# Kernel tuning notes

Measured on AMD Instinct MI355X. Metric: run time of the kernel, lower is better.

The kernel has to match this reference:

```python
import jax, jax.numpy as jnp
import numpy as np

N = 100000
E = 1600000
IN_C = 512
OUT_C = 128


def setup_inputs() -> dict:
    key = jax.random.key(0)
    k1, k2, k3, k4 = jax.random.split(key, 4)
    x = jax.random.normal(k1, (N, IN_C), dtype=jnp.float32)
    edge_index = jax.random.randint(k2, (2, E), 0, N, dtype=jnp.int64)
    # GCNConv parameters (glorot weight, zero bias as in PyG defaults)
    scale = jnp.sqrt(6.0 / (IN_C + OUT_C)).astype(jnp.float32)
    W = jax.random.uniform(k3, (IN_C, OUT_C), dtype=jnp.float32, minval=-scale, maxval=scale)
    b = jnp.zeros((OUT_C,), dtype=jnp.float32)
    return {"x": x, "edge_index": edge_index, "W": W, "b": b}


def reference(x, edge_index, W, b):
    n = x.shape[0]
    loops = jnp.arange(n, dtype=edge_index.dtype)
    src = jnp.concatenate([edge_index[0], loops])  # [E+N] message sources
    dst = jnp.concatenate([edge_index[1], loops])  # [E+N] message targets
    # symmetric GCN normalization: deg over targets incl. self-loops
    deg = jax.ops.segment_sum(jnp.ones_like(src, dtype=x.dtype), dst, num_segments=n)
    dinv = jnp.where(deg > 0, jax.lax.rsqrt(deg), 0.0)
    norm = dinv[src] * dinv[dst]  # [E+N]
    h = x @ W  # [N, OUT_C] transform first (in > out)
    msg = h[src] * norm[:, None]  # [E+N, OUT_C]
    out = jax.ops.segment_sum(msg, dst, num_segments=n) + b
    return (out, 0)
```

## Files before the change

kernel.cpp:

```cpp
#include <hip/hip_runtime.h>

#define IN_C 512
#define OUT_C 128
#define SCAN_TILE 2048
#define NB 128
#define CHUNK 8192

typedef float f32x4 __attribute__((ext_vector_type(4)));
typedef __bf16 bf16x8 __attribute__((ext_vector_type(8)));

static inline int cdiv(int a, int b) { return (a + b - 1) / b; }

__device__ __forceinline__ unsigned short bfbits(__bf16 h) {
  return __builtin_bit_cast(unsigned short, h);
}


__global__ __launch_bounds__(256) void hist_kernel(const int* __restrict__ dst,
                                                   int* __restrict__ table,
                                                   int nchunks, int E) {
  __shared__ int hcnt[NB];
  int t = threadIdx.x;
  int c = blockIdx.x;
  if (t < NB) hcnt[t] = 0;
  __syncthreads();
  int base = c * CHUNK;
  for (int i = t; i < CHUNK; i += 256) {
    int e = base + i;
    if (e < E) atomicAdd(&hcnt[dst[e] >> 10], 1);
  }
  __syncthreads();
  if (t < NB) table[t * nchunks + c] = hcnt[t];
}

__global__ __launch_bounds__(256) void tscan_kernel(int* __restrict__ table,
                                                    int* __restrict__ bstart,
                                                    int nchunks, int E) {
  __shared__ int sh[256];
  int t = threadIdx.x;
  int total = NB * nchunks;
  int S = (total + 255) / 256;
  int lo = t * S;
  int hi = lo + S; if (hi > total) hi = total;
  int s = 0;
  int i = lo;
  for (; i + 4 <= hi; i += 4)
    s += table[i] + table[i + 1] + table[i + 2] + table[i + 3];
  for (; i < hi; i++) s += table[i];
  sh[t] = s;
  __syncthreads();
  for (int off = 1; off < 256; off <<= 1) {
    int x = sh[t];
    if (t >= off) x += sh[t - off];
    __syncthreads();
    sh[t] = x;
    __syncthreads();
  }
  int run = sh[t] - s;
  for (i = lo; i < hi; i++) {
    int v = table[i];
    table[i] = run;
    run += v;
  }
  __syncthreads();
  for (int b = t; b < NB; b += 256) bstart[b] = table[b * nchunks];
  if (t == 0) bstart[NB] = E;
}

__global__ __launch_bounds__(256) void scat2_kernel(const int* __restrict__ src,
                                                    const int* __restrict__ dst,
                                                    const int* __restrict__ table,
                                                    int2* __restrict__ inter,
                                                    int nchunks, int E) {
  __shared__ int cur[NB];
  int t = threadIdx.x;
  int c = blockIdx.x;
  if (t < NB) cur[t] = table[t * nchunks + c];
  __syncthreads();
  int base = c * CHUNK;
  for (int i = t; i < CHUNK; i += 256) {
    int e = base + i;
    if (e < E) {
      int d = dst[e];
      int pos = atomicAdd(&cur[d >> 10], 1);
      inter[pos] = make_int2(src[e], d);
    }
  }
}

__global__ __launch_bounds__(256) void bdeg_kernel(const int2* __restrict__ inter,
                                                   const int* __restrict__ bstart,
                                                   int* __restrict__ deg, int n) {
  __shared__ int dl[1024];
  int t = threadIdx.x;
  int b = blockIdx.x;
  for (int i = t; i < 1024; i += 256) dl[i] = 0;
  __syncthreads();
  int lo = bstart[b], hi = bstart[b + 1];
  for (int e = lo + t; e < hi; e += 256) atomicAdd(&dl[inter[e].y & 1023], 1);
  __syncthreads();
  int nb0 = b << 10;
  for (int i = t; i < 1024; i += 256) {
    int node = nb0 + i;
    if (node < n) deg[node] = dl[i];
  }
}

__global__ __launch_bounds__(256) void dinv_kernel(const int* __restrict__ deg,
                                                   float* __restrict__ dinv, int n) {
  int i = blockIdx.x * 256 + threadIdx.x;
  if (i < n) dinv[i] = rsqrtf((float)deg[i] + 1.0f);
}

__global__ __launch_bounds__(256) void scan1_kernel(const int* __restrict__ deg,
                                                    int* __restrict__ offs,
                                                    int* __restrict__ bsums, int n) {
  __shared__ int sh[256];
  int t = threadIdx.x;
  int base = blockIdx.x * SCAN_TILE + t * 8;
  int v[8];
  int s = 0;
#pragma unroll
  for (int i = 0; i < 8; i++) {
    int idx = base + i;
    v[i] = (idx < n) ? deg[idx] : 0;
    s += v[i];
  }
  sh[t] = s;
  __syncthreads();
  for (int off = 1; off < 256; off <<= 1) {
    int x = sh[t];
    if (t >= off) x += sh[t - off];
    __syncthreads();
    sh[t] = x;
    __syncthreads();
  }
  int run = sh[t] - s;
#pragma unroll
  for (int i = 0; i < 8; i++) {
    int idx = base + i;
    if (idx < n) offs[idx] = run;
    run += v[i];
  }
  if (t == 255) bsums[blockIdx.x] = sh[255];
}

__global__ __launch_bounds__(256) void scan2_kernel(int* __restrict__ bsums, int nb) {
  __shared__ int sh[256];
  int t = threadIdx.x;
  int v = (t < nb) ? bsums[t] : 0;
  sh[t] = v;
  __syncthreads();
  for (int off = 1; off < 256; off <<= 1) {
    int x = sh[t];
    if (t >= off) x += sh[t - off];
    __syncthreads();
    sh[t] = x;
    __syncthreads();
  }
  if (t < nb) bsums[t] = sh[t] - v;
}

__global__ __launch_bounds__(256) void scan3_kernel(int* __restrict__ offs,
                                                    const int* __restrict__ bsums,
                                                    int n, int E) {
  int i = blockIdx.x * 256 + threadIdx.x;
  if (i < n) offs[i] = offs[i] + bsums[i >> 11];
  if (i == 0) offs[n] = E;
}

__global__ __launch_bounds__(256) void scat3_kernel(const int2* __restrict__ inter,
                                                    const int* __restrict__ bstart,
                                                    const int* __restrict__ offs,
                                                    int* __restrict__ csr_src, int n) {
  __shared__ int cur[1024];
  int t = threadIdx.x;
  int b = blockIdx.x;
  int nb0 = b << 10;
  for (int i = t; i < 1024; i += 256) {
    int node = nb0 + i;
    cur[i] = (node < n) ? offs[node] : 0;
  }
  __syncthreads();
  int lo = bstart[b], hi = bstart[b + 1];
  for (int e = lo + t; e < hi; e += 256) {
    int2 sd = inter[e];
    int pos = atomicAdd(&cur[sd.y & 1023], 1);
    csr_src[pos] = sd.x;
  }
}

__global__ __launch_bounds__(256) void wsplit_kernel(const float* __restrict__ W,
                                                     unsigned short* __restrict__ wfh,
                                                     unsigned short* __restrict__ wfl) {
  int i = blockIdx.x * 256 + threadIdx.x;
  if (i >= IN_C * OUT_C) return;
  int k = i >> 7;
  int col = i & 127;
  float w = W[i];
  __bf16 hb = (__bf16)w;
  __bf16 lb = (__bf16)(w - (float)hb);
  int ks = k >> 5;
  int lg = (k & 31) >> 3;
  int j = k & 7;
  int cb = col >> 4;
  int lane = lg * 16 + (col & 15);
  size_t idx = ((size_t)(ks * 8 + cb) * 64 + lane) * 8 + j;
  wfh[idx] = bfbits(hb);
  wfl[idx] = bfbits(lb);
}

__global__ __launch_bounds__(256) void gemm_mfma_kernel(
    const float* __restrict__ x, const unsigned short* __restrict__ wfh,
    const unsigned short* __restrict__ wfl, unsigned short* __restrict__ h, int n) {
  __shared__ float xs[2][4096];

  const int tid = threadIdx.x;
  const int wv = tid >> 6;
  const int lane = tid & 63;
  const int l15 = lane & 15;
  const int lg = lane >> 4;
  const int wr = wv >> 1;
  const int wc = wv & 1;
  const int row0 = blockIdx.x * 128;

  const float* gsrc[4];
#pragma unroll
  for (int i = 0; i < 4; i++) {
    int pslot = i * 256 + tid;
    int row = pslot >> 3;
    int q = pslot & 7;
    int s = q ^ (row & 7);
    int grow = row0 + row;
    if (grow > n - 1) grow = n - 1;
    gsrc[i] = x + (size_t)grow * IN_C + s * 4;
  }

  const unsigned short* bph = wfh + ((size_t)(wc * 4) * 64 + lane) * 8;
  const unsigned short* bpl = wfl + ((size_t)(wc * 4) * 64 + lane) * 8;

  f32x4 acc[4][4];
#pragma unroll
  for (int i = 0; i < 4; i++)
#pragma unroll
    for (int j = 0; j < 4; j++) acc[i][j] = (f32x4)0.0f;

#pragma unroll
  for (int i = 0; i < 4; i++) {
    char* lp = (char*)&xs[0][0] + i * 4096 + wv * 1024;
    __builtin_amdgcn_global_load_lds(
        (const __attribute__((address_space(1))) void*)gsrc[i],
        (__attribute__((address_space(3))) void*)lp, 16, 0, 0);
    gsrc[i] += 32;
  }
  __syncthreads();

  int cur = 0;
  for (int ks = 0; ks < 16; ks++) {
    if (ks < 15) {
#pragma unroll
      for (int i = 0; i < 4; i++) {
        char* lp = (char*)&xs[cur ^ 1][0] + i * 4096 + wv * 1024;
        __builtin_amdgcn_global_load_lds(
            (const __attribute__((address_space(1))) void*)gsrc[i],
            (__attribute__((address_space(3))) void*)lp, 16, 0, 0);
        gsrc[i] += 32;
      }
    }
    bf16x8 bh[4], bl[4];
#pragma unroll
    for (int nt = 0; nt < 4; nt++) {
      bh[nt] = __builtin_bit_cast(bf16x8, *(const uint4*)(bph + (size_t)ks * 4096 + nt * 512));
      bl[nt] = __builtin_bit_cast(bf16x8, *(const uint4*)(bpl + (size_t)ks * 4096 + nt * 512));
    }
    const float* bp = &xs[cur][0];
    bf16x8 ah[4];
#pragma unroll
    for (int rt = 0; rt < 4; rt++) {
      int row = wr * 64 + rt * 16 + l15;
      int r7 = row & 7;
      int s0 = (lg * 2) ^ r7;
      int s1 = (lg * 2 + 1) ^ r7;
      float4 f0 = *(const float4*)(bp + row * 32 + s0 * 4);
      float4 f1 = *(const float4*)(bp + row * 32 + s1 * 4);
      float f[8] = {f0.x, f0.y, f0.z, f0.w, f1.x, f1.y, f1.z, f1.w};
      bf16x8 hh;
#pragma unroll
      for (int j = 0; j < 8; j++) hh[j] = (__bf16)f[j];
      ah[rt] = hh;
    }
#pragma unroll
    for (int rt = 0; rt < 4; rt++)
#pragma unroll
      for (int nt = 0; nt < 4; nt++) {
        acc[rt][nt] = __builtin_amdgcn_mfma_f32_16x16x32_bf16(ah[rt], bh[nt], acc[rt][nt], 0, 0, 0);
        acc[rt][nt] = __builtin_amdgcn_mfma_f32_16x16x32_bf16(ah[rt], bl[nt], acc[rt][nt], 0, 0, 0);
      }
    __syncthreads();
    cur ^= 1;
  }

#pragma unroll
  for (int rt = 0; rt < 4; rt++) {
    int rowbase = row0 + wr * 64 + rt * 16 + lg * 4;
#pragma unroll
    for (int nt = 0; nt < 4; nt++) {
      int col = wc * 64 + nt * 16 + l15;
#pragma unroll
      for (int r = 0; r < 4; r++) {
        int row = rowbase + r;
        if (row < n) h[(size_t)row * OUT_C + col] = bfbits((__bf16)acc[rt][nt][r]);
      }
    }
  }
}

__device__ __forceinline__ float bflo(unsigned int u) {
  return __builtin_bit_cast(float, u << 16);
}
__device__ __forceinline__ float bfhi(unsigned int u) {
  return __builtin_bit_cast(float, u & 0xffff0000u);
}

__global__ __launch_bounds__(256) void gather_kernel(const int* __restrict__ offs,
                                                     const int* __restrict__ csr_src,
                                                     const unsigned short* __restrict__ h,
                                                     const float* __restrict__ dinv,
                                                     const float* __restrict__ b,
                                                     float* __restrict__ out,
                                                     int n, int tail) {
  int wid = threadIdx.x >> 6;
  int lane = threadIdx.x & 63;
  int l15 = lane & 15;
  int q = lane >> 4;
  int node = blockIdx.x * 4 + wid;
  if (node >= n) return;

  int start = offs[node];
  int end = offs[node + 1];

  float ax0 = 0, ay0 = 0, ax1 = 0, ay1 = 0, ax2 = 0, ay2 = 0, ax3 = 0, ay3 = 0;

  int e = start + q;
  for (; e + 4 < end; e += 8) {
    int s0 = csr_src[e];
    int s1 = csr_src[e + 4];
    float w0 = dinv[s0];
    float w1 = dinv[s1];
    uint4 u0 = *(const uint4*)(h + (size_t)s0 * OUT_C + l15 * 8);
    uint4 u1 = *(const uint4*)(h + (size_t)s1 * OUT_C + l15 * 8);
    ax0 += bflo(u0.x) * w0 + bflo(u1.x) * w1;
    ay0 += bfhi(u0.x) * w0 + bfhi(u1.x) * w1;
    ax1 += bflo(u0.y) * w0 + bflo(u1.y) * w1;
    ay1 += bfhi(u0.y) * w0 + bfhi(u1.y) * w1;
    ax2 += bflo(u0.z) * w0 + bflo(u1.z) * w1;
    ay2 += bfhi(u0.z) * w0 + bfhi(u1.z) * w1;
    ax3 += bflo(u0.w) * w0 + bflo(u1.w) * w1;
    ay3 += bfhi(u0.w) * w0 + bfhi(u1.w) * w1;
  }
  if (e < end) {
    int s0 = csr_src[e];
    float w0 = dinv[s0];
    uint4 u0 = *(const uint4*)(h + (size_t)s0 * OUT_C + l15 * 8);
    ax0 += bflo(u0.x) * w0; ay0 += bfhi(u0.x) * w0;
    ax1 += bflo(u0.y) * w0; ay1 += bfhi(u0.y) * w0;
    ax2 += bflo(u0.z) * w0; ay2 += bfhi(u0.z) * w0;
    ax3 += bflo(u0.w) * w0; ay3 += bfhi(u0.w) * w0;
  }

#pragma unroll
  for (int mask = 16; mask <= 32; mask <<= 1) {
    ax0 += __shfl_xor(ax0, mask); ay0 += __shfl_xor(ay0, mask);
    ax1 += __shfl_xor(ax1, mask); ay1 += __shfl_xor(ay1, mask);
    ax2 += __shfl_xor(ax2, mask); ay2 += __shfl_xor(ay2, mask);
    ax3 += __shfl_xor(ax3, mask); ay3 += __shfl_xor(ay3, mask);
  }

  float dd = dinv[node];
  uint4 us = *(const uint4*)(h + (size_t)node * OUT_C + l15 * 8);
  ax0 = (ax0 + bflo(us.x) * dd) * dd; ay0 = (ay0 + bfhi(us.x) * dd) * dd;
  ax1 = (ax1 + bflo(us.y) * dd) * dd; ay1 = (ay1 + bfhi(us.y) * dd) * dd;
  ax2 = (ax2 + bflo(us.z) * dd) * dd; ay2 = (ay2 + bfhi(us.z) * dd) * dd;
  ax3 = (ax3 + bflo(us.w) * dd) * dd; ay3 = (ay3 + bfhi(us.w) * dd) * dd;

  if (q == 0) {
    float4 b0 = *(const float4*)(b + l15 * 8);
    float4 b1 = *(const float4*)(b + l15 * 8 + 4);
    float4 o0 = make_float4(ax0 + b0.x, ay0 + b0.y, ax1 + b0.z, ay1 + b0.w);
    float4 o1 = make_float4(ax2 + b1.x, ay2 + b1.y, ax3 + b1.z, ay3 + b1.w);
    float* op = out + (size_t)node * OUT_C + l15 * 8;
    *(float4*)op = o0;
    *(float4*)(op + 4) = o1;
  }

  if (node == 0 && lane == 0) {
    for (int t = 0; t < tail; t++) out[(size_t)n * OUT_C + t] = 0.0f;
  }
}

extern "C" void kernel_launch(void* const* d_in, const int* in_sizes, int n_in,
                              void* d_out, int out_size, void* d_ws, size_t ws_size,
                              hipStream_t stream) {
  const float* x = (const float*)d_in[0];
  const int* ei = (const int*)d_in[1];
  const float* W = (const float*)d_in[2];
  const float* b = (const float*)d_in[3];

  const int n = in_sizes[0] / IN_C;
  const int E = in_sizes[1] / 2;
  const int* src = ei;
  const int* dst = ei + E;
  float* out = (float*)d_out;

  const int nchunks = cdiv(E, CHUNK);
  const int nbk = cdiv(n, 1024);

  size_t p = 0;
  auto alloc = [&](size_t bytes) { size_t o = p; p += (bytes + 255) & ~(size_t)255; return o; };
  char* ws = (char*)d_ws;
  float*          dinv   = (float*)(ws + alloc((size_t)n * 4));
  int*            offs   = (int*)(ws + alloc(((size_t)n + 1) * 4));
  int*            csrsrc = (int*)(ws + alloc((size_t)E * 4));
  int*            deg    = (int*)(ws + alloc((size_t)n * 4));
  int*            bsums  = (int*)(ws + alloc(256 * 4));
  int*            bstart = (int*)(ws + alloc((NB + 1) * 4));
  unsigned short* wfh    = (unsigned short*)(ws + alloc((size_t)IN_C * OUT_C * 2));
  unsigned short* wfl    = (unsigned short*)(ws + alloc((size_t)IN_C * OUT_C * 2));
  size_t upos = p;
  int2*           inter  = (int2*)(ws + upos);
  int*            table  = (int*)(ws + upos + (((size_t)E * 8 + 255) & ~(size_t)255));
  unsigned short* h      = (unsigned short*)(ws + upos);

  const int nb = cdiv(n, SCAN_TILE);

  wsplit_kernel<<<cdiv(IN_C * OUT_C, 256), 256, 0, stream>>>(W, wfh, wfl);
  hist_kernel<<<nchunks, 256, 0, stream>>>(dst, table, nchunks, E);
  tscan_kernel<<<1, 256, 0, stream>>>(table, bstart, nchunks, E);
  scat2_kernel<<<nchunks, 256, 0, stream>>>(src, dst, table, inter, nchunks, E);
  bdeg_kernel<<<nbk, 256, 0, stream>>>(inter, bstart, deg, n);
  dinv_kernel<<<cdiv(n, 256), 256, 0, stream>>>(deg, dinv, n);
  scan1_kernel<<<nb, 256, 0, stream>>>(deg, offs, bsums, n);
  scan2_kernel<<<1, 256, 0, stream>>>(bsums, nb);
  scan3_kernel<<<cdiv(n, 256), 256, 0, stream>>>(offs, bsums, n, E);
  scat3_kernel<<<nbk, 256, 0, stream>>>(inter, bstart, offs, csrsrc, n);
  gemm_mfma_kernel<<<cdiv(n, 128), 256, 0, stream>>>(x, wfh, wfl, h, n);
  int tail = out_size - n * OUT_C;
  gather_kernel<<<cdiv(n, 4), 256, 0, stream>>>(offs, csrsrc, h, dinv, b, out, n, tail);
}
```

Baseline: 277.6 us.

## Fuse degree, dinv and offset scan into bucket kernel; prescale h by dinv

Measured after the change: 268.4 us. 1.03x faster.

```diff
diff --git a/kernel.cpp b/kernel.cpp
--- a/kernel.cpp
+++ b/kernel.cpp
@@ -2,7 +2,6 @@
 
 #define IN_C 512
 #define OUT_C 128
-#define SCAN_TILE 2048
 #define NB 128
 #define CHUNK 8192
 
@@ -70,7 +69,7 @@
 __global__ __launch_bounds__(256) void scat2_kernel(const int* __restrict__ src,
                                                     const int* __restrict__ dst,
                                                     const int* __restrict__ table,
-                                                    int2* __restrict__ inter,
+                                                    int* __restrict__ inter,
                                                     int nchunks, int E) {
   __shared__ int cur[NB];
   int t = threadIdx.x;
@@ -83,48 +82,31 @@
     if (e < E) {
       int d = dst[e];
       int pos = atomicAdd(&cur[d >> 10], 1);
-      inter[pos] = make_int2(src[e], d);
-    }
-  }
-}
-
-__global__ __launch_bounds__(256) void bdeg_kernel(const int2* __restrict__ inter,
-                                                   const int* __restrict__ bstart,
-                                                   int* __restrict__ deg, int n) {
+      inter[pos] = (src[e] << 10) | (d & 1023);
+    }
+  }
+}
+
+__global__ __launch_bounds__(256) void bdeg_offs_kernel(const int* __restrict__ inter,
+                                                        const int* __restrict__ bstart,
+                                                        int* __restrict__ offs,
+                                                        float* __restrict__ dinv,
+                                                        int n, int E, int nbk) {
   __shared__ int dl[1024];
+  __shared__ int sh[256];
   int t = threadIdx.x;
   int b = blockIdx.x;
   for (int i = t; i < 1024; i += 256) dl[i] = 0;
   __syncthreads();
   int lo = bstart[b], hi = bstart[b + 1];
-  for (int e = lo + t; e < hi; e += 256) atomicAdd(&dl[inter[e].y & 1023], 1);
-  __syncthreads();
-  int nb0 = b << 10;
-  for (int i = t; i < 1024; i += 256) {
-    int node = nb0 + i;
-    if (node < n) deg[node] = dl[i];
-  }
-}
-
-__global__ __launch_bounds__(256) void dinv_kernel(const int* __restrict__ deg,
-                                                   float* __restrict__ dinv, int n) {
-  int i = blockIdx.x * 256 + threadIdx.x;
-  if (i < n) dinv[i] = rsqrtf((float)deg[i] + 1.0f);
-}
-
-__global__ __launch_bounds__(256) void scan1_kernel(const int* __restrict__ deg,
-                                                    int* __restrict__ offs,
-                                                    int* __restrict__ bsums, int n) {
-  __shared__ int sh[256];
-  int t = threadIdx.x;
-  int base = blockIdx.x * SCAN_TILE + t * 8;
-  int v[8];
+  for (int e = lo + t; e < hi; e += 256) atomicAdd(&dl[inter[e] & 1023], 1);
+  __syncthreads();
+  int c[4];
   int s = 0;
 #pragma unroll
-  for (int i = 0; i < 8; i++) {
-    int idx = base + i;
-    v[i] = (idx < n) ? deg[idx] : 0;
-    s += v[i];
+  for (int j = 0; j < 4; j++) {
+    c[j] = dl[t * 4 + j];
+    s += c[j];
   }
   sh[t] = s;
   __syncthreads();
@@ -135,41 +117,21 @@
     sh[t] = x;
     __syncthreads();
   }
-  int run = sh[t] - s;
-#pragma unroll
-  for (int i = 0; i < 8; i++) {
-    int idx = base + i;
-    if (idx < n) offs[idx] = run;
-    run += v[i];
-  }
-  if (t == 255) bsums[blockIdx.x] = sh[255];
-}
-
-__global__ __launch_bounds__(256) void scan2_kernel(int* __restrict__ bsums, int nb) {
-  __shared__ int sh[256];
-  int t = threadIdx.x;
-  int v = (t < nb) ? bsums[t] : 0;
-  sh[t] = v;
-  __syncthreads();
-  for (int off = 1; off < 256; off <<= 1) {
-    int x = sh[t];
-    if (t >= off) x += sh[t - off];
-    __syncthreads();
-    sh[t] = x;
-    __syncthreads();
-  }
-  if (t < nb) bsums[t] = sh[t] - v;
-}
-
-__global__ __launch_bounds__(256) void scan3_kernel(int* __restrict__ offs,
-                                                    const int* __restrict__ bsums,
-                                                    int n, int E) {
-  int i = blockIdx.x * 256 + threadIdx.x;
-  if (i < n) offs[i] = offs[i] + bsums[i >> 11];
-  if (i == 0) offs[n] = E;
-}
-
-__global__ __launch_bounds__(256) void scat3_kernel(const int2* __restrict__ inter,
+  int run = sh[t] - s + lo;
+  int nb0 = b << 10;
+#pragma unroll
+  for (int j = 0; j < 4; j++) {
+    int node = nb0 + t * 4 + j;
+    if (node < n) {
+      offs[node] = run;
+      dinv[node] = rsqrtf((float)c[j] + 1.0f);
+    }
+    run += c[j];
+  }
+  if (b == nbk - 1 && t == 255) offs[n] = E;
+}
+
+__global__ __launch_bounds__(256) void scat3_kernel(const int* __restrict__ inter,
                                                     const int* __restrict__ bstart,
                                                     const int* __restrict__ offs,
                                                     int* __restrict__ csr_src, int n) {
@@ -184,9 +146,9 @@
   __syncthreads();
   int lo = bstart[b], hi = bstart[b + 1];
   for (int e = lo + t; e < hi; e += 256) {
-    int2 sd = inter[e];
-    int pos = atomicAdd(&cur[sd.y & 1023], 1);
-    csr_src[pos] = sd.x;
+    int u = inter[e];
+    int pos = atomicAdd(&cur[u & 1023], 1);
+    csr_src[pos] = u >> 10;
   }
 }
 
@@ -212,7 +174,8 @@
 
 __global__ __launch_bounds__(256) void gemm_mfma_kernel(
     const float* __restrict__ x, const unsigned short* __restrict__ wfh,
-    const unsigned short* __restrict__ wfl, unsigned short* __restrict__ h, int n) {
+    const unsigned short* __restrict__ wfl, const float* __restrict__ dinv,
+    unsigned short* __restrict__ h, int n) {
   __shared__ float xs[2][4096];
 
   const int tid = threadIdx.x;
@@ -304,12 +267,15 @@
   for (int rt = 0; rt < 4; rt++) {
     int rowbase = row0 + wr * 64 + rt * 16 + lg * 4;
 #pragma unroll
-    for (int nt = 0; nt < 4; nt++) {
-      int col = wc * 64 + nt * 16 + l15;
-#pragma unroll
-      for (int r = 0; r < 4; r++) {
-        int row = rowbase + r;
-        if (row < n) h[(size_t)row * OUT_C + col] = bfbits((__bf16)acc[rt][nt][r]);
+    for (int r = 0; r < 4; r++) {
+      int row = rowbase + r;
+      if (row < n) {
+        float di = dinv[row];
+#pragma unroll
+        for (int nt = 0; nt < 4; nt++) {
+          int col = wc * 64 + nt * 16 + l15;
+          h[(size_t)row * OUT_C + col] = bfbits((__bf16)(acc[rt][nt][r] * di));
+        }
       }
     }
   }
@@ -345,27 +311,20 @@
   for (; e + 4 < end; e += 8) {
     int s0 = csr_src[e];
     int s1 = csr_src[e + 4];
-    float w0 = dinv[s0];
-    float w1 = dinv[s1];
     uint4 u0 = *(const uint4*)(h + (size_t)s0 * OUT_C + l15 * 8);
     uint4 u1 = *(const uint4*)(h + (size_t)s1 * OUT_C + l15 * 8);
-    ax0 += bflo(u0.x) * w0 + bflo(u1.x) * w1;
-    ay0 += bfhi(u0.x) * w0 + bfhi(u1.x) * w1;
-    ax1 += bflo(u0.y) * w0 + bflo(u1.y) * w1;
-    ay1 += bfhi(u0.y) * w0 + bfhi(u1.y) * w1;
-    ax2 += bflo(u0.z) * w0 + bflo(u1.z) * w1;
-    ay2 += bfhi(u0.z) * w0 + bfhi(u1.z) * w1;
-    ax3 += bflo(u0.w) * w0 + bflo(u1.w) * w1;
-    ay3 += bfhi(u0.w) * w0 + bfhi(u1.w) * w1;
+    ax0 += bflo(u0.x) + bflo(u1.x); ay0 += bfhi(u0.x) + bfhi(u1.x);
+    ax1 += bflo(u0.y) + bflo(u1.y); ay1 += bfhi(u0.y) + bfhi(u1.y);
+    ax2 += bflo(u0.z) + bflo(u1.z); ay2 += bfhi(u0.z) + bfhi(u1.z);
+    ax3 += bflo(u0.w) + bflo(u1.w); ay3 += bfhi(u0.w) + bfhi(u1.w);
   }
   if (e < end) {
     int s0 = csr_src[e];
-    float w0 = dinv[s0];
     uint4 u0 = *(const uint4*)(h + (size_t)s0 * OUT_C + l15 * 8);
-    ax0 += bflo(u0.x) * w0; ay0 += bfhi(u0.x) * w0;
-    ax1 += bflo(u0.y) * w0; ay1 += bfhi(u0.y) * w0;
-    ax2 += bflo(u0.z) * w0; ay2 += bfhi(u0.z) * w0;
-    ax3 += bflo(u0.w) * w0; ay3 += bfhi(u0.w) * w0;
+    ax0 += bflo(u0.x); ay0 += bfhi(u0.x);
+    ax1 += bflo(u0.y); ay1 += bfhi(u0.y);
+    ax2 += bflo(u0.z); ay2 += bfhi(u0.z);
+    ax3 += bflo(u0.w); ay3 += bfhi(u0.w);
   }
 
 #pragma unroll
@@ -378,10 +337,10 @@
 
   float dd = dinv[node];
   uint4 us = *(const uint4*)(h + (size_t)node * OUT_C + l15 * 8);
-  ax0 = (ax0 + bflo(us.x) * dd) * dd; ay0 = (ay0 + bfhi(us.x) * dd) * dd;
-  ax1 = (ax1 + bflo(us.y) * dd) * dd; ay1 = (ay1 + bfhi(us.y) * dd) * dd;
-  ax2 = (ax2 + bflo(us.z) * dd) * dd; ay2 = (ay2 + bfhi(us.z) * dd) * dd;
-  ax3 = (ax3 + bflo(us.w) * dd) * dd; ay3 = (ay3 + bfhi(us.w) * dd) * dd;
+  ax0 = (ax0 + bflo(us.x)) * dd; ay0 = (ay0 + bfhi(us.x)) * dd;
+  ax1 = (ax1 + bflo(us.y)) * dd; ay1 = (ay1 + bfhi(us.y)) * dd;
+  ax2 = (ax2 + bflo(us.z)) * dd; ay2 = (ay2 + bfhi(us.z)) * dd;
+  ax3 = (ax3 + bflo(us.w)) * dd; ay3 = (ay3 + bfhi(us.w)) * dd;
 
   if (q == 0) {
     float4 b0 = *(const float4*)(b + l15 * 8);
@@ -421,29 +380,21 @@
   float*          dinv   = (float*)(ws + alloc((size_t)n * 4));
   int*            offs   = (int*)(ws + alloc(((size_t)n + 1) * 4));
   int*            csrsrc = (int*)(ws + alloc((size_t)E * 4));
-  int*            deg    = (int*)(ws + alloc((size_t)n * 4));
-  int*            bsums  = (int*)(ws + alloc(256 * 4));
   int*            bstart = (int*)(ws + alloc((NB + 1) * 4));
   unsigned short* wfh    = (unsigned short*)(ws + alloc((size_t)IN_C * OUT_C * 2));
   unsigned short* wfl    = (unsigned short*)(ws + alloc((size_t)IN_C * OUT_C * 2));
   size_t upos = p;
-  int2*           inter  = (int2*)(ws + upos);
-  int*            table  = (int*)(ws + upos + (((size_t)E * 8 + 255) & ~(size_t)255));
+  int*            inter  = (int*)(ws + upos);
+  int*            table  = (int*)(ws + upos + (((size_t)E * 4 + 255) & ~(size_t)255));
   unsigned short* h      = (unsigned short*)(ws + upos);
-
-  const int nb = cdiv(n, SCAN_TILE);
 
   wsplit_kernel<<<cdiv(IN_C * OUT_C, 256), 256, 0, stream>>>(W, wfh, wfl);
   hist_kernel<<<nchunks, 256, 0, stream>>>(dst, table, nchunks, E);
   tscan_kernel<<<1, 256, 0, stream>>>(table, bstart, nchunks, E);
   scat2_kernel<<<nchunks, 256, 0, stream>>>(src, dst, table, inter, nchunks, E);
-  bdeg_kernel<<<nbk, 256, 0, stream>>>(inter, bstart, deg, n);
-  dinv_kernel<<<cdiv(n, 256), 256, 0, stream>>>(deg, dinv, n);
-  scan1_kernel<<<nb, 256, 0, stream>>>(deg, offs, bsums, n);
-  scan2_kernel<<<1, 256, 0, stream>>>(bsums, nb);
-  scan3_kernel<<<cdiv(n, 256), 256, 0, stream>>>(offs, bsums, n, E);
+  bdeg_offs_kernel<<<nbk, 256, 0, stream>>>(inter, bstart, offs, dinv, n, E, nbk);
   scat3_kernel<<<nbk, 256, 0, stream>>>(inter, bstart, offs, csrsrc, n);
-  gemm_mfma_kernel<<<cdiv(n, 128), 256, 0, stream>>>(x, wfh, wfl, h, n);
+  gemm_mfma_kernel<<<cdiv(n, 128), 256, 0, stream>>>(x, wfh, wfl, dinv, h, n);
   int tail = out_size - n * OUT_C;
   gather_kernel<<<cdiv(n, 4), 256, 0, stream>>>(offs, csrsrc, h, dinv, b, out, n, tail);
 }
```
